# Performance work log

Hardware: AMD Instinct MI355X
Metric: run time of the kernel (lower is better)

Reference implementation:

```python
import math
import jax, jax.numpy as jnp
import numpy as np
from jax import lax

B, T, D, S, N_SLOTS, N_ITERS = 16, 4096, 768, 768, 16, 8
THR, EPS = 0.5, 1e-8
SCALE = D ** -0.5
NEG = -jnp.finfo(jnp.float32).max


def ln(x, g, b):
    mu = x.mean(-1, keepdims=True)
    var = ((x - mu) ** 2).mean(-1, keepdims=True)
    return (x - mu) / jnp.sqrt(var + 1e-5) * g + b


def gru_cell(u, h, wih, whh, bih, bhh):
    # torch GRUCell: r,z,n gate ordering
    gi = u @ wih.T + bih
    gh = h @ whh.T + bhh
    ir, iz, inn = jnp.split(gi, 3, axis=-1)
    hr, hz, hn = jnp.split(gh, 3, axis=-1)
    r = jax.nn.sigmoid(ir + hr)
    z = jax.nn.sigmoid(iz + hz)
    n = jnp.tanh(inn + r * hn)
    return (1.0 - z) * n + z * h


def sa_step(slots, k, v, p, slot_mask, context_mask):
    q = ln(slots, p['lsg'], p['lsb']) @ p['Wq'].T
    dots = jnp.einsum('bid,bjd->bij', q, k) * SCALE  # [B, n_slots, T]
    dots = jnp.where(context_mask[:, None, :], dots, NEG)
    if slot_mask is not None:
        dots = jnp.where(slot_mask[:, :, None], dots, NEG)
    attn_vis = jax.nn.softmax(dots, axis=1)  # softmax over SLOTS (inverted attn)
    attn = attn_vis + EPS
    attn = attn / attn.sum(-1, keepdims=True)
    updates = jnp.einsum('bjd,bij->bid', v, attn)
    b, n, d = slots.shape
    h = gru_cell(updates.reshape(b * n, d), slots.reshape(b * n, d),
                 p['gwih'], p['gwhh'], p['gbih'], p['gbhh'])
    slots = h.reshape(b, n, d)
    pre = ln(slots, p['lfg'], p['lfb'])
    slots = slots + (jax.nn.relu(pre @ p['w1'].T + p['b1']) @ p['w2'].T + p['b2'])
    return slots, attn_vis


def cluster_single(slots, attn, slot_mask):
    sl = lax.stop_gradient(slots)  # torch no_grad block
    ns = sl / jnp.clip(jnp.linalg.norm(sl, axis=-1, keepdims=True), 1e-12)
    smm = (slot_mask[:, :, None] & slot_mask[:, None, :]).astype(jnp.float32)
    dist = 1.0 - jnp.einsum('bnd,bmd->bnm', ns, ns)
    dist = jnp.where(smm > 0, dist, 2.0)
    adj = (dist < THR).astype(jnp.float32) * smm
    for _ in range(math.ceil(math.log2(N_SLOTS))):  # transitive closure by squaring
        adj = jnp.minimum(adj @ adj, 1.0) * smm
    cum = jnp.cumsum(adj, axis=1)
    cm = adj * (cum <= 1.0)  # keep first row of each connected component
    counts = (cm > 0).any(axis=2).sum(axis=1)
    reset = counts < 3
    eye = jnp.eye(N_SLOTS, dtype=jnp.float32)[None] * slot_mask[:, :, None].astype(jnp.float32)
    cm = jnp.where(reset[:, None, None], eye, cm)
    cw = cm / jnp.clip(cm.sum(axis=2, keepdims=True), 1.0)
    cm = lax.stop_gradient(cm)
    cw = lax.stop_gradient(cw)
    means = cw @ slots          # grads flow through slots only
    cattn = cm @ attn           # grads flow through attn only
    out_mask = (cm > 0).any(axis=2) & slot_mask
    return means, cattn, out_mask


def setup_inputs() -> dict:
    key = jax.random.key(0)
    ks = jax.random.split(key, 16)
    sc = 0.02
    return {
        'x': jax.random.normal(ks[0], (B, T, D), jnp.float32),
        'context_mask': jnp.ones((B, T), jnp.bool_),
        'n_slots': N_SLOTS,
        'slots_init': jax.random.normal(ks[1], (N_SLOTS, S), jnp.float32),
        'Wk': jax.random.normal(ks[2], (S, D), jnp.float32) * sc,
        'Wv': jax.random.normal(ks[3], (S, D), jnp.float32) * sc,
        'Wq': jax.random.normal(ks[4], (S, S), jnp.float32) * sc,
        'gwih': jax.random.normal(ks[5], (3 * S, S), jnp.float32) * sc,
        'gwhh': jax.random.normal(ks[6], (3 * S, S), jnp.float32) * sc,
        'gbih': jnp.zeros((3 * S,), jnp.float32),
        'gbhh': jnp.zeros((3 * S,), jnp.float32),
        'w1': jax.random.normal(ks[7], (4 * S, S), jnp.float32) * sc,
        'b1': jnp.zeros((4 * S,), jnp.float32),
        'w2': jax.random.normal(ks[8], (S, 4 * S), jnp.float32) * sc,
        'b2': jnp.zeros((S,), jnp.float32),
        'lin_g': jnp.ones((D,), jnp.float32), 'lin_b': jnp.zeros((D,), jnp.float32),
        'lsg': jnp.ones((S,), jnp.float32), 'lsb': jnp.zeros((S,), jnp.float32),
        'lfg': jnp.ones((S,), jnp.float32), 'lfb': jnp.zeros((S,), jnp.float32),
    }


def reference(x, context_mask, n_slots, slots_init, Wk, Wv, Wq, gwih, gwhh,
              gbih, gbhh, w1, b1, w2, b2, lin_g, lin_b, lsg, lsb, lfg, lfb):
    p = dict(Wq=Wq, gwih=gwih, gwhh=gwhh, gbih=gbih, gbhh=gbhh,
             w1=w1, b1=b1, w2=w2, b2=b2, lsg=lsg, lsb=lsb, lfg=lfg, lfb=lfb)
    xn = ln(x, lin_g, lin_b)
    init_slots = jnp.broadcast_to(slots_init[None], (x.shape[0], N_SLOTS, S))
    k = xn @ Wk.T
    v = xn @ Wv.T
    slots = init_slots
    for _ in range(N_ITERS):
        slots, attn = sa_step(slots, k, v, p, None, context_mask)
    # implicit differentiation trick
    slots = lax.stop_gradient(slots) - lax.stop_gradient(init_slots) + init_slots
    slot_mask = jnp.ones((x.shape[0], N_SLOTS), jnp.bool_)
    slots, attn = sa_step(slots, k, v, p, slot_mask, context_mask)
    slots, attn, slot_mask = cluster_single(slots, attn, slot_mask)
    attn_map = jnp.transpose(attn, (0, 2, 1))  # [B, T, n_slots]
    return slots, attn_map, slot_mask
```

## Files before the change

kernel.cpp:

```cpp
#include <hip/hip_runtime.h>
#include <hip/hip_bf16.h>

typedef __hip_bfloat16 bf16;
typedef __attribute__((ext_vector_type(4))) float f32x4;
typedef __attribute__((ext_vector_type(8))) short s16x8;
typedef unsigned int u32;
typedef unsigned short u16;

#define B_ 16
#define T_ 4096
#define D_ 768
#define S_ 768
#define NS 16
#define NIT 9
#define NCHUNK 16
#define TCH 256
#define EPS 1e-8f
#define SCALE 0.036084391824351615f

__device__ __forceinline__ void gld16(const void* g, void* l) {
    __builtin_amdgcn_global_load_lds((const __attribute__((address_space(1))) u32*)g,
                                     (__attribute__((address_space(3))) u32*)l, 16, 0, 0);
}

__device__ __forceinline__ u16 bfbits(float x) {
    bf16 h = __float2bfloat16(x);
    return *reinterpret_cast<u16*>(&h);
}

__global__ void __launch_bounds__(256) cvt_all_kernel(
    const float* __restrict__ wq, const float* __restrict__ wk, const float* __restrict__ wv,
    const float* __restrict__ gwih, const float* __restrict__ gwhh,
    const float* __restrict__ w1, const float* __restrict__ w2,
    bf16* __restrict__ wq_b, bf16* __restrict__ wkv_b,
    bf16* __restrict__ gwih_b, bf16* __restrict__ gwhh_b,
    bf16* __restrict__ w1_b, bf16* __restrict__ w2_b)
{
    int i = blockIdx.x * 256 + threadIdx.x;
    const int NW = 589824, NG = 1769472, NM = 2359296;
    if (i < NW) { wq_b[i] = __float2bfloat16(wq[i]); return; }
    i -= NW;
    if (i < NW) { wkv_b[i] = __float2bfloat16(wk[i]); return; }
    i -= NW;
    if (i < NW) { wkv_b[NW + i] = __float2bfloat16(wv[i]); return; }
    i -= NW;
    if (i < NG) { gwih_b[i] = __float2bfloat16(gwih[i]); return; }
    i -= NG;
    if (i < NG) { gwhh_b[i] = __float2bfloat16(gwhh[i]); return; }
    i -= NG;
    if (i < NM) { w1_b[i] = __float2bfloat16(w1[i]); return; }
    i -= NM;
    w2_b[i] = __float2bfloat16(w2[i]);
}

__global__ void __launch_bounds__(256) ln768_kernel(
    const float* __restrict__ x, const float* __restrict__ g,
    const float* __restrict__ bta, bf16* __restrict__ out)
{
    int row = blockIdx.x;
    int tid = threadIdx.x;
    const float* xr = x + (size_t)row * 768;
    float v0 = xr[tid], v1 = xr[tid + 256], v2 = xr[tid + 512];
    float s = v0 + v1 + v2;
    int lane = tid & 63, wid = tid >> 6;
    #pragma unroll
    for (int off = 32; off; off >>= 1) s += __shfl_down(s, off);
    __shared__ float red[4];
    __shared__ float sh_mu, sh_rs;
    if (lane == 0) red[wid] = s;
    __syncthreads();
    if (tid == 0) sh_mu = (red[0] + red[1] + red[2] + red[3]) * (1.f / 768.f);
    __syncthreads();
    float mu = sh_mu;
    float d0 = v0 - mu, d1 = v1 - mu, d2 = v2 - mu;
    float q = d0 * d0 + d1 * d1 + d2 * d2;
    #pragma unroll
    for (int off = 32; off; off >>= 1) q += __shfl_down(q, off);
    if (lane == 0) red[wid] = q;
    __syncthreads();
    if (tid == 0) sh_rs = rsqrtf((red[0] + red[1] + red[2] + red[3]) * (1.f / 768.f) + 1e-5f);
    __syncthreads();
    float rs = sh_rs;
    bf16* orow = out + (size_t)row * 768;
    orow[tid]       = __float2bfloat16(d0 * rs * g[tid]       + bta[tid]);
    orow[tid + 256] = __float2bfloat16(d1 * rs * g[tid + 256] + bta[tid + 256]);
    orow[tid + 512] = __float2bfloat16(d2 * rs * g[tid + 512] + bta[tid + 512]);
}

__global__ void __launch_bounds__(512) gemm256_kernel(
    const bf16* __restrict__ A, const bf16* __restrict__ W,
    bf16* __restrict__ kout, bf16* __restrict__ vTout, float* __restrict__ vsum)
{
    __shared__ char smem[49152];
    __shared__ float vs_l[128];
    bf16* As = (bf16*)smem;
    bf16* Bs = (bf16*)(smem + 32768);
    int tid = threadIdx.x, lane = tid & 63, wid = tid >> 6;
    int bid = blockIdx.x;
    int xcd = bid & 7, idx = bid >> 3;
    int mt = xcd * 32 + idx / 12;
    int nt = idx % 12;
    int bm0 = mt * 256, bn0 = nt * 128;
    int wr = wid >> 1, wc = wid & 1;
    int g = lane >> 4, r15 = lane & 15;
    const f32x4 vzero = {0.f, 0.f, 0.f, 0.f};
    f32x4 acc[4][4];
    #pragma unroll
    for (int m = 0; m < 4; ++m)
        #pragma unroll
        for (int n = 0; n < 4; ++n) acc[m][n] = vzero;

    for (int kt = 0; kt < 768; kt += 64) {
        __syncthreads();
        #pragma unroll
        for (int i = 0; i < 4; ++i) {
            int s0 = i * 512 + wid * 64;
            int o = (s0 + lane) * 16;
            int r = o >> 7, cb = o & 127;
            int cbs = cb ^ ((r & 7) << 4);
            gld16(A + (size_t)(bm0 + r) * 768 + kt + (cbs >> 1), (char*)As + (size_t)s0 * 16);
        }
        #pragma unroll
        for (int i = 0; i < 2; ++i) {
            int s0 = i * 512 + wid * 64;
            int o = (s0 + lane) * 16;
            int r = o >> 7, cb = o & 127;
            int cbs = cb ^ ((r & 7) << 4);
            gld16(W + (size_t)(bn0 + r) * 768 + kt + (cbs >> 1), (char*)Bs + (size_t)s0 * 16);
        }
        asm volatile("s_waitcnt vmcnt(0)" ::: "memory");
        __syncthreads();
        #pragma unroll
        for (int kk2 = 0; kk2 < 2; ++kk2) {
            s16x8 af[4], bfr[4];
            #pragma unroll
            for (int m = 0; m < 4; ++m) {
                int r = wr * 64 + m * 16 + r15;
                int p = r * 128 + ((kk2 * 64 + g * 16) ^ ((r & 7) << 4));
                af[m] = *(const s16x8*)((const char*)As + p);
            }
            #pragma unroll
            for (int n = 0; n < 4; ++n) {
                int r = wc * 64 + n * 16 + r15;
                int p = r * 128 + ((kk2 * 64 + g * 16) ^ ((r & 7) << 4));
                bfr[n] = *(const s16x8*)((const char*)Bs + p);
            }
            #pragma unroll
            for (int m = 0; m < 4; ++m)
                #pragma unroll
                for (int n = 0; n < 4; ++n)
                    acc[m][n] = __builtin_amdgcn_mfma_f32_16x16x32_bf16(af[m], bfr[n], acc[m][n], 0, 0, 0);
        }
    }

    bool is_v = (bn0 >= 768);
    float* Ct = (float*)smem;
    int bq = bm0 >> 12;
    int tloc = bm0 & 4095;
    if (is_v && tid < 128) vs_l[tid] = 0.f;
    #pragma unroll
    for (int q = 0; q < 4; ++q) {
        __syncthreads();
        if (wr == q) {
            #pragma unroll
            for (int m = 0; m < 4; ++m)
                #pragma unroll
                for (int n = 0; n < 4; ++n)
                    #pragma unroll
                    for (int j = 0; j < 4; ++j)
                        Ct[(m * 16 + g * 4 + j) * 132 + wc * 64 + n * 16 + r15] = acc[m][n][j];
        }
        __syncthreads();
        if (!is_v) {
            int r = tid >> 3, cq = tid & 7;
            u16 tmp[16];
            #pragma unroll
            for (int i = 0; i < 16; ++i) tmp[i] = bfbits(Ct[r * 132 + cq * 16 + i]);
            s16x8 o0, o1;
            #pragma unroll
            for (int i = 0; i < 8; ++i) { o0[i] = (short)tmp[i]; o1[i] = (short)tmp[8 + i]; }
            bf16* dst = kout + (size_t)(bm0 + q * 64 + r) * 768 + bn0 + cq * 16;
            *(s16x8*)dst = o0;
            *(s16x8*)(dst + 8) = o1;
        } else {
            int d = tid >> 2, tq = tid & 3;
            float ssum = 0.f;
            u16 tmp[16];
            #pragma unroll
            for (int i = 0; i < 16; ++i) {
                float f = Ct[(tq * 16 + i) * 132 + d];
                ssum += f;
                tmp[i] = bfbits(f);
            }
            s16x8 o0, o1;
            #pragma unroll
            for (int i = 0; i < 8; ++i) { o0[i] = (short)tmp[i]; o1[i] = (short)tmp[8 + i]; }
            bf16* dst = vTout + ((size_t)bq * 768 + (bn0 - 768) + d) * (size_t)T_
                        + tloc + q * 64 + tq * 16;
            *(s16x8*)dst = o0;
            *(s16x8*)(dst + 8) = o1;
            atomicAdd(&vs_l[d], ssum);
        }
    }
    if (is_v) {
        __syncthreads();
        if (tid < 128) atomicAdd(vsum + bq * 768 + (bn0 - 768) + tid, vs_l[tid]);
    }
}

__global__ void init_slots_kernel(const float* __restrict__ si,
                                  float* __restrict__ slots, bf16* __restrict__ slots_bf)
{
    int idx = blockIdx.x * 256 + threadIdx.x;
    float v = si[idx % (NS * S_)];
    slots[idx] = v;
    slots_bf[idx] = __float2bfloat16(v);
}

__global__ void __launch_bounds__(256) ln_gemm_kernel(
    const float* __restrict__ xin, const float* __restrict__ gam, const float* __restrict__ bet,
    const bf16* __restrict__ W, const float* __restrict__ bias,
    bf16* __restrict__ out, int N, int relu)
{
    __shared__ bf16 As[16 * 768];
    __shared__ bf16 Ws[2][64 * 64];
    int tid = threadIdx.x;
    int bx = blockIdx.x, bn0 = blockIdx.y * 64;
    int row = tid >> 4, li = tid & 15;
    const float* xr = xin + (size_t)(bx * 16 + row) * 768;
    float vals[48];
    float s = 0.f;
    #pragma unroll
    for (int i = 0; i < 48; ++i) { vals[i] = xr[li + i * 16]; s += vals[i]; }
    #pragma unroll
    for (int m = 1; m < 16; m <<= 1) s += __shfl_xor(s, m);
    float mu = s * (1.f / 768.f);
    float q = 0.f;
    #pragma unroll
    for (int i = 0; i < 48; ++i) { float d = vals[i] - mu; q += d * d; }
    #pragma unroll
    for (int m = 1; m < 16; m <<= 1) q += __shfl_xor(q, m);
    float rs = rsqrtf(q * (1.f / 768.f) + 1e-5f);
    #pragma unroll
    for (int i = 0; i < 48; ++i) {
        int c = li + i * 16;
        float v = (vals[i] - mu) * rs * gam[c] + bet[c];
        *(u16*)((char*)As + row * 1536 + ((c * 2) ^ ((row & 7) << 4))) = bfbits(v);
    }
    int lane = tid & 63, wid = tid >> 6;
    int g = lane >> 4, s15 = lane & 15;
    auto stageW = [&](int kt, int buf) {
        #pragma unroll
        for (int i = 0; i < 2; ++i) {
            int s0 = i * 256 + wid * 64;
            int o = (s0 + lane) * 16;
            int r = o >> 7, cb = o & 127;
            int cbs = cb ^ ((r & 7) << 4);
            gld16(W + (size_t)(bn0 + r) * 768 + kt + (cbs >> 1),
                  (char*)Ws[buf] + (size_t)s0 * 16);
        }
    };
    stageW(0, 0);
    asm volatile("s_waitcnt vmcnt(0)" ::: "memory");
    __syncthreads();
    f32x4 acc = {0.f, 0.f, 0.f, 0.f};
    int rb = wid * 16 + s15;
    for (int t = 0; t < 12; ++t) {
        int cur = t & 1;
        if (t < 11) stageW((t + 1) * 64, cur ^ 1);
        #pragma unroll
        for (int kk2 = 0; kk2 < 2; ++kk2) {
            int kabs = t * 64 + kk2 * 32;
            s16x8 af = *(const s16x8*)((const char*)As + s15 * 1536 +
                                       ((kabs * 2 + g * 16) ^ ((s15 & 7) << 4)));
            s16x8 bf_ = *(const s16x8*)((const char*)Ws[cur] + rb * 128 +
                                        ((kk2 * 64 + g * 16) ^ ((rb & 7) << 4)));
            acc = __builtin_amdgcn_mfma_f32_16x16x32_bf16(af, bf_, acc, 0, 0, 0);
        }
        asm volatile("s_waitcnt vmcnt(0)" ::: "memory");
        __syncthreads();
    }
    int cn = bn0 + rb;
    float bv = bias ? bias[cn] : 0.f;
    #pragma unroll
    for (int j = 0; j < 4; ++j) {
        float val = acc[j] + bv;
        if (relu) val = fmaxf(val, 0.f);
        out[(size_t)(bx * 16 + g * 4 + j) * N + cn] = __float2bfloat16(val);
    }
}

__device__ __forceinline__ void skinny_body(
    const bf16* A, const bf16* Bm, const float* bias, const float* Cin,
    float* Cf, bf16* Cb, int N, int K, int bm0, int bn0, int relu,
    bf16* As, bf16* Bs)
{
    int tid = threadIdx.x, lane = tid & 63, wid = tid >> 6;
    int g = lane >> 4, r15 = lane & 15;
    f32x4 acc = {0.f, 0.f, 0.f, 0.f};
    for (int kt = 0; kt < K; kt += 64) {
        __syncthreads();
        #pragma unroll
        for (int i = 0; i < 3; ++i) {
            int s0 = i * 256 + wid * 64;
            if (s0 < 640) {
                int o = (s0 + lane) * 16;
                if (o < 2048) {
                    int r = o >> 7, cb = o & 127;
                    int cbs = cb ^ ((r & 7) << 4);
                    gld16(A + (size_t)(bm0 + r) * K + kt + (cbs >> 1), (char*)As + (size_t)s0 * 16);
                } else {
                    int ob = o - 2048;
                    int r = ob >> 7, cb = ob & 127;
                    int cbs = cb ^ ((r & 7) << 4);
                    gld16(Bm + (size_t)(bn0 + r) * K + kt + (cbs >> 1),
                          (char*)Bs + (size_t)(s0 * 16 - 2048));
                }
            }
        }
        asm volatile("s_waitcnt vmcnt(0)" ::: "memory");
        __syncthreads();
        #pragma unroll
        for (int kk = 0; kk < 64; kk += 32) {
            int pa = r15 * 128 + ((kk * 2 + g * 16) ^ ((r15 & 7) << 4));
            s16x8 af = *(const s16x8*)((const char*)As + pa);
            int rb = wid * 16 + r15;
            int pb = rb * 128 + ((kk * 2 + g * 16) ^ ((rb & 7) << 4));
            s16x8 bfr = *(const s16x8*)((const char*)Bs + pb);
            acc = __builtin_amdgcn_mfma_f32_16x16x32_bf16(af, bfr, acc, 0, 0, 0);
        }
    }
    int cn = bn0 + wid * 16 + r15;
    float bv = bias ? bias[cn] : 0.f;
    #pragma unroll
    for (int j = 0; j < 4; ++j) {
        int cm = bm0 + g * 4 + j;
        size_t ci = (size_t)cm * N + cn;
        float val = acc[j] + bv;
        if (Cin) val += Cin[ci];
        if (relu) val = fmaxf(val, 0.f);
        if (Cf) Cf[ci] = val;
        if (Cb) Cb[ci] = __float2bfloat16(val);
    }
}

__global__ void __launch_bounds__(256) mlp2_kernel(
    const bf16* __restrict__ h1, const bf16* __restrict__ W2, const float* __restrict__ b2,
    const float* __restrict__ slotsB, float* __restrict__ slotsA, bf16* __restrict__ slotsA_bf)
{
    __shared__ bf16 As[16 * 64];
    __shared__ bf16 Bs[64 * 64];
    skinny_body(h1, W2, b2, slotsB, slotsA, slotsA_bf, 768, 3072,
                blockIdx.x * 16, blockIdx.y * 64, 0, As, Bs);
}

__global__ void __launch_bounds__(256) gru_gemm_kernel(
    const bf16* __restrict__ upd, const bf16* __restrict__ slots_bf,
    const bf16* __restrict__ Wih, const bf16* __restrict__ Whh,
    const float* __restrict__ bih, const float* __restrict__ bhh,
    float* __restrict__ gi, float* __restrict__ gh)
{
    __shared__ bf16 As[16 * 64];
    __shared__ bf16 Bs[64 * 64];
    int y = blockIdx.y;
    if (y < 36)
        skinny_body(upd, Wih, bih, nullptr, gi, nullptr, 2304, 768,
                    blockIdx.x * 16, y * 64, 0, As, Bs);
    else
        skinny_body(slots_bf, Whh, bhh, nullptr, gh, nullptr, 2304, 768,
                    blockIdx.x * 16, (y - 36) * 64, 0, As, Bs);
}

__global__ void __launch_bounds__(256) fused_attn_kernel(
    const bf16* __restrict__ q_bf, const bf16* __restrict__ k_bf, const bf16* __restrict__ vT,
    float* __restrict__ pU, float* __restrict__ prs, float* __restrict__ avis, int write_avis)
{
    __shared__ char smem[131072];
    bf16* ks0 = (bf16*)smem;
    bf16* ks1 = (bf16*)(smem + 49152);
    bf16* qs  = (bf16*)(smem + 98304);
    char* aL  = smem + 122880;
    __shared__ float rsw[2][16];
    int tid = threadIdx.x, lane = tid & 63, wid = tid >> 6;
    int b = blockIdx.x >> 4, chunk = blockIdx.x & 15;
    int t0 = chunk * TCH;
    int g = lane >> 4, s15 = lane & 15;
    const bf16* qb  = q_bf + (size_t)b * 16 * 768;
    const bf16* kb  = k_bf + (size_t)b * T_ * 768;
    const bf16* vtb = vT + (size_t)b * 768 * T_;

    auto stage_k = [&](int tb, bf16* dst) {
        #pragma unroll
        for (int i = 0; i < 12; ++i) {
            int s0 = i * 256 + wid * 64;
            int o = (s0 + lane) * 16;
            int r = o / 1536, cb = o % 1536;
            int cbs = cb ^ ((r & 7) << 4);
            gld16(kb + (size_t)(tb + r) * 768 + (cbs >> 1), (char*)dst + (size_t)s0 * 16);
        }
    };
    auto stage_v = [&](int tb, bf16* dst) {
        #pragma unroll
        for (int i = 0; i < 12; ++i) {
            int s0 = i * 256 + wid * 64;
            int o = (s0 + lane) * 16;
            int d = o >> 6, cb = o & 63;
            int cbs = cb ^ ((d & 3) << 4);
            gld16(vtb + (size_t)d * T_ + tb + (cbs >> 1), (char*)dst + (size_t)s0 * 16);
        }
    };

    #pragma unroll
    for (int i = 0; i < 6; ++i) {
        int s0 = i * 256 + wid * 64;
        int o = (s0 + lane) * 16;
        int r = o / 1536, cb = o % 1536;
        int cbs = cb ^ ((r & 7) << 4);
        gld16(qb + (size_t)r * 768 + (cbs >> 1), (char*)qs + (size_t)s0 * 16);
    }
    stage_k(t0, ks0);
    asm volatile("s_waitcnt vmcnt(0)" ::: "memory");
    __syncthreads();

    const f32x4 vzero = {0.f, 0.f, 0.f, 0.f};
    float rs_acc = 0.f;

    for (int ts = 0; ts < 8; ++ts) {
        bf16* cur = (ts & 1) ? ks1 : ks0;
        bf16* nxt = (ts & 1) ? ks0 : ks1;
        if (ts < 7) stage_k(t0 + (ts + 1) * 32, nxt);
        if (wid < 2) {
            f32x4 dacc = vzero;
            #pragma unroll
            for (int kk = 0; kk < 768; kk += 32) {
                int rk = wid * 16 + s15;
                int pk = rk * 1536 + ((kk * 2 + g * 16) ^ ((rk & 7) << 4));
                s16x8 kf = *(const s16x8*)((const char*)cur + pk);
                int pq = s15 * 1536 + ((kk * 2 + g * 16) ^ ((s15 & 7) << 4));
                s16x8 qf = *(const s16x8*)((const char*)qs + pq);
                dacc = __builtin_amdgcn_mfma_f32_16x16x32_bf16(kf, qf, dacc, 0, 0, 0);
            }
            float d0 = dacc[0] * SCALE, d1 = dacc[1] * SCALE,
                  d2 = dacc[2] * SCALE, d3 = dacc[3] * SCALE;
            float m0 = d0, m1 = d1, m2 = d2, m3 = d3;
            #pragma unroll
            for (int off = 1; off < 16; off <<= 1) {
                m0 = fmaxf(m0, __shfl_xor(m0, off));
                m1 = fmaxf(m1, __shfl_xor(m1, off));
                m2 = fmaxf(m2, __shfl_xor(m2, off));
                m3 = fmaxf(m3, __shfl_xor(m3, off));
            }
            float e0 = expf(d0 - m0), e1 = expf(d1 - m1), e2 = expf(d2 - m2), e3 = expf(d3 - m3);
            float q0 = e0, q1 = e1, q2 = e2, q3 = e3;
            #pragma unroll
            for (int off = 1; off < 16; off <<= 1) {
                q0 += __shfl_xor(q0, off);
                q1 += __shfl_xor(q1, off);
                q2 += __shfl_xor(q2, off);
                q3 += __shfl_xor(q3, off);
            }
            float a0 = e0 / q0, a1 = e1 / q1, a2 = e2 / q2, a3 = e3 / q3;
            rs_acc += a0 + a1 + a2 + a3;
            int tl = wid * 16 + g * 4;
            ushort2 p0, p1;
            p0.x = bfbits(a0); p0.y = bfbits(a1);
            p1.x = bfbits(a2); p1.y = bfbits(a3);
            int sw = (s15 & 3) << 4;
            char* aS = aL + ts * 1024;
            *(ushort2*)(aS + s15 * 64 + ((tl * 2) ^ sw))       = p0;
            *(ushort2*)(aS + s15 * 64 + (((tl + 2) * 2) ^ sw)) = p1;
            if (write_avis) {
                f32x4 w = {a0, a1, a2, a3};
                *(f32x4*)(avis + (size_t)(b * 16 + s15) * T_ + t0 + ts * 32 + tl) = w;
            }
        }
        asm volatile("s_waitcnt vmcnt(0)" ::: "memory");
        __syncthreads();
    }

    f32x4 uacc[12];
    #pragma unroll
    for (int i = 0; i < 12; ++i) uacc[i] = vzero;
    stage_v(t0, ks0);
    asm volatile("s_waitcnt vmcnt(0)" ::: "memory");
    __syncthreads();
    for (int ts = 0; ts < 8; ++ts) {
        bf16* cur = (ts & 1) ? ks1 : ks0;
        bf16* nxt = (ts & 1) ? ks0 : ks1;
        if (ts < 7) stage_v(t0 + (ts + 1) * 32, nxt);
        {
            int pa = ts * 1024 + s15 * 64 + ((g * 16) ^ ((s15 & 3) << 4));
            s16x8 afr = *(const s16x8*)(aL + pa);
            #pragma unroll
            for (int i = 0; i < 12; ++i) {
                int d = (wid * 12 + i) * 16 + s15;
                int pv = d * 64 + ((g * 16) ^ ((d & 3) << 4));
                s16x8 vf = *(const s16x8*)((const char*)cur + pv);
                uacc[i] = __builtin_amdgcn_mfma_f32_16x16x32_bf16(vf, afr, uacc[i], 0, 0, 0);
            }
        }
        asm volatile("s_waitcnt vmcnt(0)" ::: "memory");
        __syncthreads();
    }

    float* pUb = pU + (size_t)(b * 16 + chunk) * 768 * 16;
    #pragma unroll
    for (int i = 0; i < 12; ++i) {
        int dbase = (wid * 12 + i) * 16 + g * 4;
        #pragma unroll
        for (int j = 0; j < 4; ++j)
            pUb[(size_t)(dbase + j) * 16 + s15] = uacc[i][j];
    }
    rs_acc += __shfl_xor(rs_acc, 16);
    rs_acc += __shfl_xor(rs_acc, 32);
    if (wid < 2 && lane < 16) rsw[wid][s15] = rs_acc;
    __syncthreads();
    if (tid < 16) prs[(b * 16 + chunk) * 16 + tid] = rsw[0][tid] + rsw[1][tid];
}

__global__ void __launch_bounds__(256) attn_reduce_kernel(
    const float* __restrict__ pU, const float* __restrict__ prs,
    const float* __restrict__ vsum, bf16* __restrict__ upd)
{
    int idx = blockIdx.x * 256 + threadIdx.x;
    int d = idx % 768;
    int s = (idx / 768) & 15;
    int b = idx / (768 * 16);
    float su = 0.f;
    #pragma unroll
    for (int c = 0; c < 16; ++c) su += pU[((size_t)(b * 16 + c) * 768 + d) * 16 + s];
    float rs = 0.f;
    #pragma unroll
    for (int c = 0; c < 16; ++c) rs += prs[(b * 16 + c) * 16 + s];
    float val = (su + EPS * vsum[b * 768 + d]) / (rs + T_ * EPS);
    upd[idx] = __float2bfloat16(val);
}

__global__ void __launch_bounds__(256) gru_gates_kernel(
    const float* __restrict__ gi, const float* __restrict__ gh,
    const float* __restrict__ slotsA, float* __restrict__ slotsB)
{
    int idx = blockIdx.x * 256 + threadIdx.x;
    int r = idx / 768, c = idx - r * 768;
    const float* gir = gi + (size_t)r * 2304;
    const float* ghr = gh + (size_t)r * 2304;
    float ir = gir[c], iz = gir[768 + c], inn = gir[1536 + c];
    float hr = ghr[c], hz = ghr[768 + c], hn  = ghr[1536 + c];
    float rg = 1.f / (1.f + expf(-(ir + hr)));
    float z  = 1.f / (1.f + expf(-(iz + hz)));
    float n  = tanhf(inn + rg * hn);
    float h  = slotsA[idx];
    slotsB[idx] = (1.f - z) * n + z * h;
}

__global__ void __launch_bounds__(256) cluster_kernel(
    const float* __restrict__ slots, float* __restrict__ out_slots,
    float* __restrict__ out_mask, float* __restrict__ cm_g)
{
    int b = blockIdx.x;
    __shared__ float s[16][768];
    __shared__ float inv[16];
    __shared__ float adj[16][16], tmp[16][16], cw[16][16];
    __shared__ int reset_s;
    const float* sb = slots + (size_t)b * 16 * 768;
    for (int i = threadIdx.x; i < 16 * 768; i += 256) s[i / 768][i % 768] = sb[i];
    __syncthreads();
    if (threadIdx.x < 16) {
        float q = 0.f;
        for (int d = 0; d < 768; ++d) q += s[threadIdx.x][d] * s[threadIdx.x][d];
        inv[threadIdx.x] = 1.f / fmaxf(sqrtf(q), 1e-12f);
    }
    __syncthreads();
    int n = threadIdx.x >> 4, m = threadIdx.x & 15;
    float dot = 0.f;
    for (int d = 0; d < 768; ++d) dot += s[n][d] * s[m][d];
    dot *= inv[n] * inv[m];
    adj[n][m] = ((1.f - dot) < 0.5f) ? 1.f : 0.f;
    __syncthreads();
    #pragma unroll
    for (int it = 0; it < 4; ++it) {
        float t = 0.f;
        #pragma unroll
        for (int j = 0; j < 16; ++j) t += adj[n][j] * adj[j][m];
        tmp[n][m] = fminf(t, 1.f);
        __syncthreads();
        adj[n][m] = tmp[n][m];
        __syncthreads();
    }
    if (threadIdx.x < 16) {
        int mm = threadIdx.x;
        float run = 0.f;
        for (int nn = 0; nn < 16; ++nn) {
            run += adj[nn][mm];
            tmp[nn][mm] = adj[nn][mm] * ((run <= 1.f) ? 1.f : 0.f);
        }
    }
    __syncthreads();
    if (threadIdx.x == 0) {
        int cnt = 0;
        for (int nn = 0; nn < 16; ++nn) {
            bool any = false;
            for (int j = 0; j < 16; ++j) any = any || (tmp[nn][j] > 0.f);
            cnt += any ? 1 : 0;
        }
        reset_s = (cnt < 3) ? 1 : 0;
    }
    __syncthreads();
    if (reset_s) tmp[n][m] = (n == m) ? 1.f : 0.f;
    __syncthreads();
    if (threadIdx.x < 16) {
        float rs = 0.f;
        for (int j = 0; j < 16; ++j) rs += tmp[threadIdx.x][j];
        rs = fmaxf(rs, 1.f);
        for (int j = 0; j < 16; ++j) cw[threadIdx.x][j] = tmp[threadIdx.x][j] / rs;
        bool any = false;
        for (int j = 0; j < 16; ++j) any = any || (tmp[threadIdx.x][j] > 0.f);
        out_mask[b * 16 + threadIdx.x] = any ? 1.f : 0.f;
    }
    cm_g[b * 256 + threadIdx.x] = tmp[n][m];
    __syncthreads();
    for (int i = threadIdx.x; i < 16 * 768; i += 256) {
        int nn = i / 768, d = i - nn * 768;
        float acc = 0.f;
        #pragma unroll
        for (int j = 0; j < 16; ++j) acc += cw[nn][j] * s[j][d];
        out_slots[(size_t)b * 16 * 768 + i] = acc;
    }
}

__global__ void __launch_bounds__(256) cattn_kernel(
    const float* __restrict__ av, const float* __restrict__ cm_g, float* __restrict__ out_attn)
{
    int b = blockIdx.y;
    int t = blockIdx.x * 256 + threadIdx.x;
    __shared__ float cm[16][16];
    cm[threadIdx.x >> 4][threadIdx.x & 15] = cm_g[b * 256 + threadIdx.x];
    __syncthreads();
    float avv[16];
    #pragma unroll
    for (int j = 0; j < 16; ++j) avv[j] = av[((size_t)b * 16 + j) * T_ + t];
    #pragma unroll
    for (int i = 0; i < 16; ++i) {
        float acc = 0.f;
        #pragma unroll
        for (int j = 0; j < 16; ++j) acc += cm[i][j] * avv[j];
        out_attn[((size_t)b * T_ + t) * 16 + i] = acc;
    }
}

extern "C" void kernel_launch(void* const* d_in, const int* in_sizes, int n_in,
                              void* d_out, int out_size, void* d_ws, size_t ws_size,
                              hipStream_t stream)
{
    const float* x    = (const float*)d_in[0];
    const float* si   = (const float*)d_in[3];
    const float* Wk   = (const float*)d_in[4];
    const float* Wv   = (const float*)d_in[5];
    const float* Wq   = (const float*)d_in[6];
    const float* gwih = (const float*)d_in[7];
    const float* gwhh = (const float*)d_in[8];
    const float* gbih = (const float*)d_in[9];
    const float* gbhh = (const float*)d_in[10];
    const float* w1   = (const float*)d_in[11];
    const float* b1   = (const float*)d_in[12];
    const float* w2   = (const float*)d_in[13];
    const float* b2   = (const float*)d_in[14];
    const float* ling = (const float*)d_in[15];
    const float* linb = (const float*)d_in[16];
    const float* lsg  = (const float*)d_in[17];
    const float* lsb  = (const float*)d_in[18];
    const float* lfg  = (const float*)d_in[19];
    const float* lfb  = (const float*)d_in[20];

    char* w = (char*)d_ws;
    size_t off = 0;
    auto alloc = [&](size_t bytes) { void* p = w + off; off += (bytes + 255) & ~(size_t)255; return p; };
    bf16* xn     = (bf16*)alloc((size_t)B_ * T_ * D_ * 2);
    bf16* k_bf   = (bf16*)alloc((size_t)B_ * T_ * S_ * 2);
    bf16* vT     = (bf16*)alloc((size_t)B_ * S_ * T_ * 2);
    float* avis  = (float*)alloc((size_t)B_ * NS * T_ * 4);
    float* pU    = (float*)alloc((size_t)B_ * NCHUNK * S_ * NS * 4);
    float* prs   = (float*)alloc((size_t)B_ * NCHUNK * NS * 4);
    float* vsum  = (float*)alloc((size_t)B_ * S_ * 4);
    float* slotsA = (float*)alloc((size_t)B_ * NS * S_ * 4);
    bf16* slotsA_bf = (bf16*)alloc((size_t)B_ * NS * S_ * 2);
    float* slotsB = (float*)alloc((size_t)B_ * NS * S_ * 4);
    bf16* q_bf   = (bf16*)alloc((size_t)B_ * NS * S_ * 2);
    bf16* upd_bf = (bf16*)alloc((size_t)B_ * NS * S_ * 2);
    float* gi    = (float*)alloc((size_t)B_ * NS * 3 * S_ * 4);
    float* gh    = (float*)alloc((size_t)B_ * NS * 3 * S_ * 4);
    bf16* h1_bf  = (bf16*)alloc((size_t)B_ * NS * 4 * S_ * 2);
    bf16* wq_bf  = (bf16*)alloc((size_t)S_ * S_ * 2);
    bf16* wkv_bf = (bf16*)alloc((size_t)1536 * D_ * 2);
    bf16* gwih_bf = (bf16*)alloc((size_t)3 * S_ * S_ * 2);
    bf16* gwhh_bf = (bf16*)alloc((size_t)3 * S_ * S_ * 2);
    bf16* w1_bf  = (bf16*)alloc((size_t)4 * S_ * S_ * 2);
    bf16* w2_bf  = (bf16*)alloc((size_t)S_ * 4 * S_ * 2);
    float* cm_g  = (float*)alloc((size_t)B_ * 256 * 4);

    float* out_slots = (float*)d_out;
    float* out_attn  = out_slots + (size_t)B_ * NS * S_;
    float* out_mask  = out_attn + (size_t)B_ * T_ * NS;

    cvt_all_kernel<<<39168, 256, 0, stream>>>(Wq, Wk, Wv, gwih, gwhh, w1, w2,
                                              wq_bf, wkv_bf, gwih_bf, gwhh_bf, w1_bf, w2_bf);

    ln768_kernel<<<B_ * T_, 256, 0, stream>>>(x, ling, linb, xn);

    (void)hipMemsetAsync(vsum, 0, (size_t)B_ * S_ * 4, stream);
    gemm256_kernel<<<3072, 512, 0, stream>>>(xn, wkv_bf, k_bf, vT, vsum);

    init_slots_kernel<<<(B_ * NS * S_) / 256, 256, 0, stream>>>(si, slotsA, slotsA_bf);

    for (int it = 0; it < NIT; ++it) {
        {
            dim3 g(16, 12);
            ln_gemm_kernel<<<g, 256, 0, stream>>>(slotsA, lsg, lsb, wq_bf, nullptr,
                                                  q_bf, 768, 0);
        }
        fused_attn_kernel<<<B_ * NCHUNK, 256, 0, stream>>>(q_bf, k_bf, vT, pU, prs, avis,
                                                           (it == NIT - 1) ? 1 : 0);
        attn_reduce_kernel<<<(B_ * NS * S_) / 256, 256, 0, stream>>>(pU, prs, vsum, upd_bf);
        {
            dim3 g(16, 72);
            gru_gemm_kernel<<<g, 256, 0, stream>>>(upd_bf, slotsA_bf, gwih_bf, gwhh_bf,
                                                   gbih, gbhh, gi, gh);
        }
        gru_gates_kernel<<<(B_ * NS * S_) / 256, 256, 0, stream>>>(gi, gh, slotsA, slotsB);
        {
            dim3 g(16, 48);
            ln_gemm_kernel<<<g, 256, 0, stream>>>(slotsB, lfg, lfb, w1_bf, b1,
                                                  h1_bf, 3072, 1);
        }
        {
            dim3 g(16, 12);
            mlp2_kernel<<<g, 256, 0, stream>>>(h1_bf, w2_bf, b2, slotsB, slotsA, slotsA_bf);
        }
    }

    cluster_kernel<<<B_, 256, 0, stream>>>(slotsA, out_slots, out_mask, cm_g);
    {
        dim3 g(T_ / 256, B_);
        cattn_kernel<<<g, 256, 0, stream>>>(avis, cm_g, out_attn);
    }
}
```

Before: 1.464 ms.

## Fuse GRU gemms with gate math, fold attn reduce into attention, retile MLP2

The GRU input and hidden gemms now run in one kernel that computes all six gate tiles per block and applies the sigmoid/tanh gate update in the epilogue, so the gi/gh intermediates and the gates kernel go away. The per-chunk attention reduction moves into the fused attention kernel: the last block per batch, found through an atomic counter, finishes the update. The MLP2 gemm uses 64x64 tiles instead of 16x64. These changes remove three launches per iteration and the fp32 gate traffic, but the small grids (48 blocks) leave most CUs idle, and the tail reduction runs serially in a single block per batch.

```diff
diff --git a/kernel.cpp b/kernel.cpp
--- a/kernel.cpp
+++ b/kernel.cpp
@@ -175,7 +175,11 @@
             int r = tid >> 3, cq = tid & 7;
             u16 tmp[16];
             #pragma unroll
-            for (int i = 0; i < 16; ++i) tmp[i] = bfbits(Ct[r * 132 + cq * 16 + i]);
+            for (int i = 0; i < 4; ++i) {
+                f32x4 vv = *(const f32x4*)&Ct[r * 132 + cq * 16 + i * 4];
+                #pragma unroll
+                for (int jj = 0; jj < 4; ++jj) tmp[i * 4 + jj] = bfbits(vv[jj]);
+            }
             s16x8 o0, o1;
             #pragma unroll
             for (int i = 0; i < 8; ++i) { o0[i] = (short)tmp[i]; o1[i] = (short)tmp[8 + i]; }
@@ -290,57 +294,82 @@
     }
 }
 
-__device__ __forceinline__ void skinny_body(
-    const bf16* A, const bf16* Bm, const float* bias, const float* Cin,
-    float* Cf, bf16* Cb, int N, int K, int bm0, int bn0, int relu,
-    bf16* As, bf16* Bs)
-{
+__global__ void __launch_bounds__(256) gru_fused_kernel(
+    const bf16* __restrict__ upd, const bf16* __restrict__ slotsA_bf,
+    const bf16* __restrict__ Wih, const bf16* __restrict__ Whh,
+    const float* __restrict__ bih, const float* __restrict__ bhh,
+    const float* __restrict__ slotsA, float* __restrict__ slotsB)
+{
+    __shared__ char sm[65536];
     int tid = threadIdx.x, lane = tid & 63, wid = tid >> 6;
     int g = lane >> 4, r15 = lane & 15;
-    f32x4 acc = {0.f, 0.f, 0.f, 0.f};
-    for (int kt = 0; kt < K; kt += 64) {
-        __syncthreads();
-        #pragma unroll
-        for (int i = 0; i < 3; ++i) {
+    int bm0 = blockIdx.x * 64, bn0 = blockIdx.y * 64;
+    const f32x4 vz = {0.f, 0.f, 0.f, 0.f};
+    f32x4 acc[6][4];
+    #pragma unroll
+    for (int gt = 0; gt < 6; ++gt)
+        #pragma unroll
+        for (int n = 0; n < 4; ++n) acc[gt][n] = vz;
+
+    for (int kt = 0; kt < 768; kt += 64) {
+        __syncthreads();
+        #pragma unroll
+        for (int i = 0; i < 16; ++i) {
             int s0 = i * 256 + wid * 64;
-            if (s0 < 640) {
-                int o = (s0 + lane) * 16;
-                if (o < 2048) {
-                    int r = o >> 7, cb = o & 127;
-                    int cbs = cb ^ ((r & 7) << 4);
-                    gld16(A + (size_t)(bm0 + r) * K + kt + (cbs >> 1), (char*)As + (size_t)s0 * 16);
-                } else {
-                    int ob = o - 2048;
-                    int r = ob >> 7, cb = ob & 127;
-                    int cbs = cb ^ ((r & 7) << 4);
-                    gld16(Bm + (size_t)(bn0 + r) * K + kt + (cbs >> 1),
-                          (char*)Bs + (size_t)(s0 * 16 - 2048));
+            int seg = s0 + lane;
+            int reg = seg >> 9;
+            int qq = seg & 511;
+            int o = qq * 16;
+            int r = o >> 7, cb = o & 127;
+            int cbs = cb ^ ((r & 7) << 4);
+            const bf16* src;
+            if (reg == 0)      src = upd       + (size_t)(bm0 + r) * 768 + kt + (cbs >> 1);
+            else if (reg == 1) src = slotsA_bf + (size_t)(bm0 + r) * 768 + kt + (cbs >> 1);
+            else {
+                int p = reg - 2;
+                if (p < 3) src = Wih + (size_t)(p * 768 + bn0 + r) * 768 + kt + (cbs >> 1);
+                else       src = Whh + (size_t)((p - 3) * 768 + bn0 + r) * 768 + kt + (cbs >> 1);
+            }
+            gld16(src, sm + (size_t)s0 * 16);
+        }
+        asm volatile("s_waitcnt vmcnt(0)" ::: "memory");
+        __syncthreads();
+        #pragma unroll
+        for (int kk2 = 0; kk2 < 2; ++kk2) {
+            int ra = wid * 16 + r15;
+            int pa = ra * 128 + ((kk2 * 64 + g * 16) ^ ((ra & 7) << 4));
+            s16x8 au = *(const s16x8*)(sm + pa);
+            s16x8 ah = *(const s16x8*)(sm + 8192 + pa);
+            #pragma unroll
+            for (int gt = 0; gt < 6; ++gt) {
+                const char* wp = sm + 16384 + gt * 8192;
+                #pragma unroll
+                for (int n = 0; n < 4; ++n) {
+                    int rb = n * 16 + r15;
+                    int pb = rb * 128 + ((kk2 * 64 + g * 16) ^ ((rb & 7) << 4));
+                    s16x8 wf = *(const s16x8*)(wp + pb);
+                    acc[gt][n] = __builtin_amdgcn_mfma_f32_16x16x32_bf16(
+                        (gt < 3) ? au : ah, wf, acc[gt][n], 0, 0, 0);
                 }
             }
         }
-        asm volatile("s_waitcnt vmcnt(0)" ::: "memory");
-        __syncthreads();
-        #pragma unroll
-        for (int kk = 0; kk < 64; kk += 32) {
-            int pa = r15 * 128 + ((kk * 2 + g * 16) ^ ((r15 & 7) << 4));
-            s16x8 af = *(const s16x8*)((const char*)As + pa);
-            int rb = wid * 16 + r15;
-            int pb = rb * 128 + ((kk * 2 + g * 16) ^ ((rb & 7) << 4));
-            s16x8 bfr = *(const s16x8*)((const char*)Bs + pb);
-            acc = __builtin_amdgcn_mfma_f32_16x16x32_bf16(af, bfr, acc, 0, 0, 0);
-        }
-    }
-    int cn = bn0 + wid * 16 + r15;
-    float bv = bias ? bias[cn] : 0.f;
-    #pragma unroll
-    for (int j = 0; j < 4; ++j) {
-        int cm = bm0 + g * 4 + j;
-        size_t ci = (size_t)cm * N + cn;
-        float val = acc[j] + bv;
-        if (Cin) val += Cin[ci];
-        if (relu) val = fmaxf(val, 0.f);
-        if (Cf) Cf[ci] = val;
-        if (Cb) Cb[ci] = __float2bfloat16(val);
+    }
+    #pragma unroll
+    for (int n = 0; n < 4; ++n) {
+        int cn = bn0 + n * 16 + r15;
+        float bir = bih[cn], biz = bih[768 + cn], bin_ = bih[1536 + cn];
+        float bhr = bhh[cn], bhz = bhh[768 + cn], bhn = bhh[1536 + cn];
+        #pragma unroll
+        for (int j = 0; j < 4; ++j) {
+            int m = bm0 + wid * 16 + g * 4 + j;
+            float ir = acc[0][n][j] + bir, iz = acc[1][n][j] + biz, inn = acc[2][n][j] + bin_;
+            float hr = acc[3][n][j] + bhr, hz = acc[4][n][j] + bhz, hn = acc[5][n][j] + bhn;
+            float rg = 1.f / (1.f + expf(-(ir + hr)));
+            float z  = 1.f / (1.f + expf(-(iz + hz)));
+            float nn = tanhf(inn + rg * hn);
+            float h  = slotsA[(size_t)m * 768 + cn];
+            slotsB[(size_t)m * 768 + cn] = (1.f - z) * nn + z * h;
+        }
     }
 }
 
@@ -348,32 +377,62 @@
     const bf16* __restrict__ h1, const bf16* __restrict__ W2, const float* __restrict__ b2,
     const float* __restrict__ slotsB, float* __restrict__ slotsA, bf16* __restrict__ slotsA_bf)
 {
-    __shared__ bf16 As[16 * 64];
-    __shared__ bf16 Bs[64 * 64];
-    skinny_body(h1, W2, b2, slotsB, slotsA, slotsA_bf, 768, 3072,
-                blockIdx.x * 16, blockIdx.y * 64, 0, As, Bs);
-}
-
-__global__ void __launch_bounds__(256) gru_gemm_kernel(
-    const bf16* __restrict__ upd, const bf16* __restrict__ slots_bf,
-    const bf16* __restrict__ Wih, const bf16* __restrict__ Whh,
-    const float* __restrict__ bih, const float* __restrict__ bhh,
-    float* __restrict__ gi, float* __restrict__ gh)
-{
-    __shared__ bf16 As[16 * 64];
-    __shared__ bf16 Bs[64 * 64];
-    int y = blockIdx.y;
-    if (y < 36)
-        skinny_body(upd, Wih, bih, nullptr, gi, nullptr, 2304, 768,
-                    blockIdx.x * 16, y * 64, 0, As, Bs);
-    else
-        skinny_body(slots_bf, Whh, bhh, nullptr, gh, nullptr, 2304, 768,
-                    blockIdx.x * 16, (y - 36) * 64, 0, As, Bs);
+    __shared__ char sm[16384];
+    int tid = threadIdx.x, lane = tid & 63, wid = tid >> 6;
+    int g = lane >> 4, r15 = lane & 15;
+    int bm0 = blockIdx.x * 64, bn0 = blockIdx.y * 64;
+    const f32x4 vz = {0.f, 0.f, 0.f, 0.f};
+    f32x4 acc[4] = {vz, vz, vz, vz};
+    for (int kt = 0; kt < 3072; kt += 64) {
+        __syncthreads();
+        #pragma unroll
+        for (int i = 0; i < 4; ++i) {
+            int s0 = i * 256 + wid * 64;
+            int seg = s0 + lane;
+            int qq = seg & 511;
+            int o = qq * 16;
+            int r = o >> 7, cb = o & 127;
+            int cbs = cb ^ ((r & 7) << 4);
+            const bf16* src = (seg < 512)
+                ? h1 + (size_t)(bm0 + r) * 3072 + kt + (cbs >> 1)
+                : W2 + (size_t)(bn0 + r) * 3072 + kt + (cbs >> 1);
+            gld16(src, sm + (size_t)s0 * 16);
+        }
+        asm volatile("s_waitcnt vmcnt(0)" ::: "memory");
+        __syncthreads();
+        #pragma unroll
+        for (int kk2 = 0; kk2 < 2; ++kk2) {
+            int ra = wid * 16 + r15;
+            int pa = ra * 128 + ((kk2 * 64 + g * 16) ^ ((ra & 7) << 4));
+            s16x8 af = *(const s16x8*)(sm + pa);
+            #pragma unroll
+            for (int n = 0; n < 4; ++n) {
+                int rb = n * 16 + r15;
+                int pb = rb * 128 + ((kk2 * 64 + g * 16) ^ ((rb & 7) << 4));
+                s16x8 bf_ = *(const s16x8*)(sm + 8192 + pb);
+                acc[n] = __builtin_amdgcn_mfma_f32_16x16x32_bf16(af, bf_, acc[n], 0, 0, 0);
+            }
+        }
+    }
+    #pragma unroll
+    for (int n = 0; n < 4; ++n) {
+        int cn = bn0 + n * 16 + r15;
+        float bv = b2[cn];
+        #pragma unroll
+        for (int j = 0; j < 4; ++j) {
+            int m = bm0 + wid * 16 + g * 4 + j;
+            size_t ci = (size_t)m * 768 + cn;
+            float val = acc[n][j] + bv + slotsB[ci];
+            slotsA[ci] = val;
+            slotsA_bf[ci] = __float2bfloat16(val);
+        }
+    }
 }
 
 __global__ void __launch_bounds__(256) fused_attn_kernel(
     const bf16* __restrict__ q_bf, const bf16* __restrict__ k_bf, const bf16* __restrict__ vT,
-    float* __restrict__ pU, float* __restrict__ prs, float* __restrict__ avis, int write_avis)
+    float* __restrict__ pU, float* __restrict__ prs, float* __restrict__ avis, int write_avis,
+    const float* __restrict__ vsum, bf16* __restrict__ upd_bf, int* __restrict__ cnt)
 {
     __shared__ char smem[131072];
     bf16* ks0 = (bf16*)smem;
@@ -381,13 +440,15 @@
     bf16* qs  = (bf16*)(smem + 98304);
     char* aL  = smem + 122880;
     __shared__ float rsw[2][16];
+    __shared__ int sh_done;
+    __shared__ float rtot[16];
     int tid = threadIdx.x, lane = tid & 63, wid = tid >> 6;
     int b = blockIdx.x >> 4, chunk = blockIdx.x & 15;
     int t0 = chunk * TCH;
     int g = lane >> 4, s15 = lane & 15;
     const bf16* qb  = q_bf + (size_t)b * 16 * 768;
     const bf16* kb  = k_bf + (size_t)b * T_ * 768;
-    const bf16* vtb = vT + (size_t)b * 768 * T_;
+    const bf16* vtb = vT + (size_t)b * 768 * (size_t)T_;
 
     auto stage_k = [&](int tb, bf16* dst) {
         #pragma unroll
@@ -470,8 +531,8 @@
             *(ushort2*)(aS + s15 * 64 + ((tl * 2) ^ sw))       = p0;
             *(ushort2*)(aS + s15 * 64 + (((tl + 2) * 2) ^ sw)) = p1;
             if (write_avis) {
-                f32x4 w = {a0, a1, a2, a3};
-                *(f32x4*)(avis + (size_t)(b * 16 + s15) * T_ + t0 + ts * 32 + tl) = w;
+                f32x4 wv = {a0, a1, a2, a3};
+                *(f32x4*)(avis + (size_t)(b * 16 + s15) * T_ + t0 + ts * 32 + tl) = wv;
             }
         }
         asm volatile("s_waitcnt vmcnt(0)" ::: "memory");
@@ -516,41 +577,31 @@
     if (wid < 2 && lane < 16) rsw[wid][s15] = rs_acc;
     __syncthreads();
     if (tid < 16) prs[(b * 16 + chunk) * 16 + tid] = rsw[0][tid] + rsw[1][tid];
-}
-
-__global__ void __launch_bounds__(256) attn_reduce_kernel(
-    const float* __restrict__ pU, const float* __restrict__ prs,
-    const float* __restrict__ vsum, bf16* __restrict__ upd)
-{
-    int idx = blockIdx.x * 256 + threadIdx.x;
-    int d = idx % 768;
-    int s = (idx / 768) & 15;
-    int b = idx / (768 * 16);
-    float su = 0.f;
-    #pragma unroll
-    for (int c = 0; c < 16; ++c) su += pU[((size_t)(b * 16 + c) * 768 + d) * 16 + s];
-    float rs = 0.f;
-    #pragma unroll
-    for (int c = 0; c < 16; ++c) rs += prs[(b * 16 + c) * 16 + s];
-    float val = (su + EPS * vsum[b * 768 + d]) / (rs + T_ * EPS);
-    upd[idx] = __float2bfloat16(val);
-}
-
-__global__ void __launch_bounds__(256) gru_gates_kernel(
-    const float* __restrict__ gi, const float* __restrict__ gh,
-    const float* __restrict__ slotsA, float* __restrict__ slotsB)
-{
-    int idx = blockIdx.x * 256 + threadIdx.x;
-    int r = idx / 768, c = idx - r * 768;
-    const float* gir = gi + (size_t)r * 2304;
-    const float* ghr = gh + (size_t)r * 2304;
-    float ir = gir[c], iz = gir[768 + c], inn = gir[1536 + c];
-    float hr = ghr[c], hz = ghr[768 + c], hn  = ghr[1536 + c];
-    float rg = 1.f / (1.f + expf(-(ir + hr)));
-    float z  = 1.f / (1.f + expf(-(iz + hz)));
-    float n  = tanhf(inn + rg * hn);
-    float h  = slotsA[idx];
-    slotsB[idx] = (1.f - z) * n + z * h;
+
+    __syncthreads();
+    __threadfence();
+    if (tid == 0) sh_done = atomicAdd(&cnt[b], 1);
+    __syncthreads();
+    if (sh_done == 15) {
+        if (tid == 0) cnt[b] = 0;
+        __threadfence();
+        if (tid < 16) {
+            float rr = 0.f;
+            #pragma unroll
+            for (int c = 0; c < 16; ++c) rr += prs[(b * 16 + c) * 16 + tid];
+            rtot[tid] = rr + T_ * EPS;
+        }
+        __syncthreads();
+        for (int ii = tid; ii < 12288; ii += 256) {
+            int d = ii % 768, s = ii / 768;
+            float su = 0.f;
+            #pragma unroll
+            for (int c = 0; c < 16; ++c)
+                su += pU[((size_t)(b * 16 + c) * 768 + d) * 16 + s];
+            upd_bf[(size_t)(b * 16 + s) * 768 + d] =
+                __float2bfloat16((su + EPS * vsum[b * 768 + d]) / rtot[s]);
+        }
+    }
 }
 
 __global__ void __launch_bounds__(256) cluster_kernel(
@@ -597,13 +648,13 @@
     }
     __syncthreads();
     if (threadIdx.x == 0) {
-        int cnt = 0;
+        int cnt2 = 0;
         for (int nn = 0; nn < 16; ++nn) {
             bool any = false;
             for (int j = 0; j < 16; ++j) any = any || (tmp[nn][j] > 0.f);
-            cnt += any ? 1 : 0;
-        }
-        reset_s = (cnt < 3) ? 1 : 0;
+            cnt2 += any ? 1 : 0;
+        }
+        reset_s = (cnt2 < 3) ? 1 : 0;
     }
     __syncthreads();
     if (reset_s) tmp[n][m] = (n == m) ? 1.f : 0.f;
@@ -682,13 +733,12 @@
     float* pU    = (float*)alloc((size_t)B_ * NCHUNK * S_ * NS * 4);
     float* prs   = (float*)alloc((size_t)B_ * NCHUNK * NS * 4);
     float* vsum  = (float*)alloc((size_t)B_ * S_ * 4);
+    int*   cnt   = (int*)alloc(B_ * 4);
     float* slotsA = (float*)alloc((size_t)B_ * NS * S_ * 4);
     bf16* slotsA_bf = (bf16*)alloc((size_t)B_ * NS * S_ * 2);
     float* slotsB = (float*)alloc((size_t)B_ * NS * S_ * 4);
     bf16* q_bf   = (bf16*)alloc((size_t)B_ * NS * S_ * 2);
     bf16* upd_bf = (bf16*)alloc((size_t)B_ * NS * S_ * 2);
-    float* gi    = (float*)alloc((size_t)B_ * NS * 3 * S_ * 4);
-    float* gh    = (float*)alloc((size_t)B_ * NS * 3 * S_ * 4);
     bf16* h1_bf  = (bf16*)alloc((size_t)B_ * NS * 4 * S_ * 2);
     bf16* wq_bf  = (bf16*)alloc((size_t)S_ * S_ * 2);
     bf16* wkv_bf = (bf16*)alloc((size_t)1536 * D_ * 2);
@@ -708,6 +758,7 @@
     ln768_kernel<<<B_ * T_, 256, 0, stream>>>(x, ling, linb, xn);
 
     (void)hipMemsetAsync(vsum, 0, (size_t)B_ * S_ * 4, stream);
+    (void)hipMemsetAsync(cnt, 0, B_ * 4, stream);
     gemm256_kernel<<<3072, 512, 0, stream>>>(xn, wkv_bf, k_bf, vT, vsum);
 
     init_slots_kernel<<<(B_ * NS * S_) / 256, 256, 0, stream>>>(si, slotsA, slotsA_bf);
@@ -719,21 +770,20 @@
                                                   q_bf, 768, 0);
         }
         fused_attn_kernel<<<B_ * NCHUNK, 256, 0, stream>>>(q_bf, k_bf, vT, pU, prs, avis,
-                                                           (it == NIT - 1) ? 1 : 0);
-        attn_reduce_kernel<<<(B_ * NS * S_) / 256, 256, 0, stream>>>(pU, prs, vsum, upd_bf);
+                                                           (it == NIT - 1) ? 1 : 0,
+                                                           vsum, upd_bf, cnt);
         {
-            dim3 g(16, 72);
-            gru_gemm_kernel<<<g, 256, 0, stream>>>(upd_bf, slotsA_bf, gwih_bf, gwhh_bf,
-                                                   gbih, gbhh, gi, gh);
-        }
-        gru_gates_kernel<<<(B_ * NS * S_) / 256, 256, 0, stream>>>(gi, gh, slotsA, slotsB);
+            dim3 g(4, 12);
+            gru_fused_kernel<<<g, 256, 0, stream>>>(upd_bf, slotsA_bf, gwih_bf, gwhh_bf,
+                                                    gbih, gbhh, slotsA, slotsB);
+        }
         {
             dim3 g(16, 48);
             ln_gemm_kernel<<<g, 256, 0, stream>>>(slotsB, lfg, lfb, w1_bf, b1,
                                                   h1_bf, 3072, 1);
         }
         {
-            dim3 g(16, 12);
+            dim3 g(4, 12);
             mlp2_kernel<<<g, 256, 0, stream>>>(h1_bf, w2_bf, b2, slotsB, slotsA, slotsA_bf);
         }
     }
```

Result: slower. 2.864 ms (+95.6%).
